# Kernel optimization log

Hardware: AMD Instinct MI355X
Metric: run time of the kernel (lower is better)

Reference implementation:

```python
import jax, jax.numpy as jnp
import numpy as np

CAPACITY_KWH = 13.5
MAX_CHARGE_RATE_KW = 5.0
INITIAL_CHARGE_KWH = 6.75
KW_TO_KWH = 5.0 / 60.0  # 5-minute interval

B, T = 4096, 4096


def setup_inputs() -> dict:
    key = jax.random.key(0)
    k1, k2, k3, k4 = jax.random.split(key, 4)
    return {
        "grid_action": jax.random.normal(k1, (B, T), dtype=jnp.float32),
        "pv_action": jax.random.uniform(k2, (B, T), dtype=jnp.float32),
        "pv_power": jax.random.uniform(k3, (B, T), dtype=jnp.float32),
        "price": jax.random.uniform(k4, (B, T), dtype=jnp.float32),
    }


def _battery_rollout(grid_action, pv_action, pv_power, price):
    # precompute per-step provisional quantities (all [B, T])
    attempted_pv_rate = pv_action * pv_power
    realised_pv_rate = jnp.clip(attempted_pv_rate, 0.0, MAX_CHARGE_RATE_KW)
    prov_pv_amount = realised_pv_rate * KW_TO_KWH
    attempted_grid_rate = grid_action * MAX_CHARGE_RATE_KW

    def step(state, inp):
        ppc, pvp, agr = inp  # each [B]
        after_pv = jnp.clip(state + ppc, 0.0, CAPACITY_KWH)
        realised_pv_amt = after_pv - state
        actual_pv_rate = realised_pv_amt / KW_TO_KWH
        pv_export = realised_pv_amt - pvp * KW_TO_KWH
        realised_grid_rate = jnp.clip(agr, -MAX_CHARGE_RATE_KW,
                                      MAX_CHARGE_RATE_KW - actual_pv_rate)
        new_state = jnp.clip(after_pv + realised_grid_rate * KW_TO_KWH,
                             0.0, CAPACITY_KWH)
        grid_amt = new_state - after_pv
        return new_state, (new_state, grid_amt, pv_export)

    init = jnp.full((grid_action.shape[0],), INITIAL_CHARGE_KWH,
                    dtype=grid_action.dtype)
    xs = (prov_pv_amount.T, pv_power.T, attempted_grid_rate.T)  # [T, B]
    _, (states, grid_amt, pv_export) = jax.lax.scan(step, init, xs)
    trace = jnp.concatenate([init[None, :], states], axis=0).T  # [B, T+1]
    cost = price / 1000.0 * (grid_amt.T + pv_export.T)          # [B, T]
    return trace, cost


def reference(grid_action, pv_action, pv_power, price):
    return _battery_rollout(grid_action, pv_action, pv_power, price)
```

## Files before the change

kernel.cpp:

```cpp
#include <hip/hip_runtime.h>

#define T_STEPS 4096
#define BLOCK   1024
#define CHUNK   4

constexpr float CAP     = 13.5f;
constexpr float MAXR    = 5.0f;
constexpr float S0      = 6.75f;
constexpr float DT      = (float)(5.0 / 60.0);
constexpr float FIVE_DT = 5.0f * DT;
constexpr float BIG     = 3.402823466e+38f;

struct Trip { float d, l, h; };

__device__ __forceinline__ Trip combine(const Trip& p, const Trip& q) {
    Trip r;
    r.d = p.d + q.d;
    r.l = fminf(fmaxf(p.l + q.d, q.l), q.h);
    r.h = fminf(fmaxf(p.h + q.d, q.l), q.h);
    return r;
}

__global__ __launch_bounds__(BLOCK) void battery_kernel(
    const float* __restrict__ ga, const float* __restrict__ pa,
    const float* __restrict__ pp, const float* __restrict__ pr,
    float* __restrict__ trace, float* __restrict__ cost)
{
    const int b    = blockIdx.x;
    const int tid  = threadIdx.x;
    const int lane = tid & 63;
    const int w    = tid >> 6;
    const long long rowOff = (long long)b * T_STEPS;
    const int t0   = tid * CHUNK;

    const float4 g4  = *reinterpret_cast<const float4*>(ga + rowOff + t0);
    const float4 pa4 = *reinterpret_cast<const float4*>(pa + rowOff + t0);
    const float4 pp4 = *reinterpret_cast<const float4*>(pp + rowOff + t0);
    const float4 pr4 = *reinterpret_cast<const float4*>(pr + rowOff + t0);
    const float gaA[4] = {g4.x,  g4.y,  g4.z,  g4.w};
    const float paA[4] = {pa4.x, pa4.y, pa4.z, pa4.w};
    const float ppA[4] = {pp4.x, pp4.y, pp4.z, pp4.w};
    const float prA[4] = {pr4.x, pr4.y, pr4.z, pr4.w};

    Trip acc;
    #pragma unroll
    for (int j = 0; j < CHUNK; ++j) {
        float rate = fminf(fmaxf(paA[j] * ppA[j], 0.0f), MAXR);
        float a    = rate * DT;
        float u    = (gaA[j] * MAXR) * DT;
        float d    = a + fminf(fmaxf(u, -FIVE_DT), FIVE_DT - a);
        float h    = fminf(fmaxf(CAP + u, CAP - FIVE_DT), CAP);
        Trip f = {d, 0.0f, h};
        acc = (j == 0) ? f : combine(acc, f);
    }

    #pragma unroll
    for (int off = 1; off < 64; off <<= 1) {
        Trip p;
        p.d = __shfl_up(acc.d, off);
        p.l = __shfl_up(acc.l, off);
        p.h = __shfl_up(acc.h, off);
        if (lane >= off) acc = combine(p, acc);
    }

    __shared__ float aggD[16], aggL[16], aggH[16];
    if (lane == 63) { aggD[w] = acc.d; aggL[w] = acc.l; aggH[w] = acc.h; }

    Trip ex;
    ex.d = __shfl_up(acc.d, 1);
    ex.l = __shfl_up(acc.l, 1);
    ex.h = __shfl_up(acc.h, 1);
    if (lane == 0) { ex.d = 0.0f; ex.l = -BIG; ex.h = BIG; }

    __syncthreads();

    Trip pre = {0.0f, -BIG, BIG};
    for (int i = 0; i < w; ++i) {
        Trip q = {aggD[i], aggL[i], aggH[i]};
        pre = combine(pre, q);
    }
    Trip tot = combine(pre, ex);
    float s = fminf(fmaxf(S0 + tot.d, tot.l), tot.h);

    float st[CHUNK], ct[CHUNK];
    #pragma unroll
    for (int j = 0; j < CHUNK; ++j) {
        float rate      = fminf(fmaxf(paA[j] * ppA[j], 0.0f), MAXR);
        float ppc       = rate * DT;
        float after_pv  = fminf(fmaxf(s + ppc, 0.0f), CAP);
        float realised  = after_pv - s;
        float apr       = realised / DT;
        float pv_export = realised - ppA[j] * DT;
        float agr       = gaA[j] * MAXR;
        float rgr       = fminf(fmaxf(agr, -MAXR), MAXR - apr);
        float ns        = fminf(fmaxf(after_pv + rgr * DT, 0.0f), CAP);
        float grid_amt  = ns - after_pv;
        st[j] = ns;
        ct[j] = (prA[j] / 1000.0f) * (grid_amt + pv_export);
        s = ns;
    }

    float4 c4; c4.x = ct[0]; c4.y = ct[1]; c4.z = ct[2]; c4.w = ct[3];
    *reinterpret_cast<float4*>(cost + rowOff + t0) = c4;

    __shared__ float tr[T_STEPS];
    float4 s4; s4.x = st[0]; s4.y = st[1]; s4.z = st[2]; s4.w = st[3];
    *reinterpret_cast<float4*>(tr + t0) = s4;
    __syncthreads();

    const long long trBase = (long long)b * (T_STEPS + 1);
    if (tid == 0) trace[trBase] = S0;
    #pragma unroll
    for (int k = 0; k < CHUNK; ++k) {
        int i = tid + k * BLOCK;
        trace[trBase + 1 + i] = tr[i];
    }
}

extern "C" void kernel_launch(void* const* d_in, const int* in_sizes, int n_in,
                              void* d_out, int out_size, void* d_ws, size_t ws_size,
                              hipStream_t stream) {
    const float* ga = (const float*)d_in[0];
    const float* pa = (const float*)d_in[1];
    const float* pp = (const float*)d_in[2];
    const float* pr = (const float*)d_in[3];
    const int B = in_sizes[0] / T_STEPS;
    float* trace = (float*)d_out;
    float* cost  = (float*)d_out + (long long)B * (T_STEPS + 1);
    battery_kernel<<<B, BLOCK, 0, stream>>>(ga, pa, pp, pr, trace, cost);
}
```

Measured before the change: 320.7 us.

## Assign one wavefront per row with tiled sequential scan and register prefetch

Instead of one 1024-thread block per row doing a block-wide scan, each 64-lane wavefront now owns a whole row. It walks the row in tiles of 512 steps, doing a wave-level scan inside each tile and carrying the state from tile to tile. The next tile's inputs are prefetched into registers, and the trace is transposed through padded per-wave LDS so stores coalesce. This removes __syncthreads and the cross-wave aggregate pass, but makes each row's work serial across tiles and raises register pressure.

After: 321.9 us. About the same (+0.4%).

```diff
diff --git a/kernel.cpp b/kernel.cpp
--- a/kernel.cpp
+++ b/kernel.cpp
@@ -1,15 +1,17 @@
 #include <hip/hip_runtime.h>
 
 #define T_STEPS 4096
-#define BLOCK   1024
-#define CHUNK   4
+#define BLOCK   256
+#define CHUNK   8
+#define TILE    (64 * CHUNK)
+#define NTILES  (T_STEPS / TILE)
+#define RPB     (BLOCK / 64)
 
 constexpr float CAP     = 13.5f;
 constexpr float MAXR    = 5.0f;
 constexpr float S0      = 6.75f;
 constexpr float DT      = (float)(5.0 / 60.0);
 constexpr float FIVE_DT = 5.0f * DT;
-constexpr float BIG     = 3.402823466e+38f;
 
 struct Trip { float d, l, h; };
 
@@ -21,99 +23,123 @@
     return r;
 }
 
-__global__ __launch_bounds__(BLOCK) void battery_kernel(
+__global__ __launch_bounds__(BLOCK, 4) void battery_kernel(
     const float* __restrict__ ga, const float* __restrict__ pa,
     const float* __restrict__ pp, const float* __restrict__ pr,
-    float* __restrict__ trace, float* __restrict__ cost)
+    float* __restrict__ trace, float* __restrict__ cost, int B)
 {
-    const int b    = blockIdx.x;
     const int tid  = threadIdx.x;
     const int lane = tid & 63;
-    const int w    = tid >> 6;
-    const long long rowOff = (long long)b * T_STEPS;
-    const int t0   = tid * CHUNK;
+    const int wv   = tid >> 6;
+    const int row  = blockIdx.x * RPB + wv;
 
-    const float4 g4  = *reinterpret_cast<const float4*>(ga + rowOff + t0);
-    const float4 pa4 = *reinterpret_cast<const float4*>(pa + rowOff + t0);
-    const float4 pp4 = *reinterpret_cast<const float4*>(pp + rowOff + t0);
-    const float4 pr4 = *reinterpret_cast<const float4*>(pr + rowOff + t0);
-    const float gaA[4] = {g4.x,  g4.y,  g4.z,  g4.w};
-    const float paA[4] = {pa4.x, pa4.y, pa4.z, pa4.w};
-    const float ppA[4] = {pp4.x, pp4.y, pp4.z, pp4.w};
-    const float prA[4] = {pr4.x, pr4.y, pr4.z, pr4.w};
+    __shared__ float buf[RPB][TILE + TILE / 8];
+    float* sb = buf[wv];
 
-    Trip acc;
-    #pragma unroll
-    for (int j = 0; j < CHUNK; ++j) {
-        float rate = fminf(fmaxf(paA[j] * ppA[j], 0.0f), MAXR);
-        float a    = rate * DT;
-        float u    = (gaA[j] * MAXR) * DT;
-        float d    = a + fminf(fmaxf(u, -FIVE_DT), FIVE_DT - a);
-        float h    = fminf(fmaxf(CAP + u, CAP - FIVE_DT), CAP);
-        Trip f = {d, 0.0f, h};
-        acc = (j == 0) ? f : combine(acc, f);
-    }
+    if (row >= B) return;
 
-    #pragma unroll
-    for (int off = 1; off < 64; off <<= 1) {
-        Trip p;
-        p.d = __shfl_up(acc.d, off);
-        p.l = __shfl_up(acc.l, off);
-        p.h = __shfl_up(acc.h, off);
-        if (lane >= off) acc = combine(p, acc);
-    }
+    const long long rowOff = (long long)row * T_STEPS;
+    const long long trBase = (long long)row * (T_STEPS + 1);
+    const float* gaR = ga + rowOff;
+    const float* paR = pa + rowOff;
+    const float* ppR = pp + rowOff;
+    const float* prR = pr + rowOff;
 
-    __shared__ float aggD[16], aggL[16], aggH[16];
-    if (lane == 63) { aggD[w] = acc.d; aggL[w] = acc.l; aggH[w] = acc.h; }
+    if (lane == 0) trace[trBase] = S0;
 
-    Trip ex;
-    ex.d = __shfl_up(acc.d, 1);
-    ex.l = __shfl_up(acc.l, 1);
-    ex.h = __shfl_up(acc.h, 1);
-    if (lane == 0) { ex.d = 0.0f; ex.l = -BIG; ex.h = BIG; }
+    const int b0 = lane * CHUNK;
+    float4 cg0 = *reinterpret_cast<const float4*>(gaR + b0);
+    float4 cg1 = *reinterpret_cast<const float4*>(gaR + b0 + 4);
+    float4 cp0 = *reinterpret_cast<const float4*>(paR + b0);
+    float4 cp1 = *reinterpret_cast<const float4*>(paR + b0 + 4);
+    float4 cq0 = *reinterpret_cast<const float4*>(ppR + b0);
+    float4 cq1 = *reinterpret_cast<const float4*>(ppR + b0 + 4);
+    float4 cr0 = *reinterpret_cast<const float4*>(prR + b0);
+    float4 cr1 = *reinterpret_cast<const float4*>(prR + b0 + 4);
 
-    __syncthreads();
+    float s = S0;
 
-    Trip pre = {0.0f, -BIG, BIG};
-    for (int i = 0; i < w; ++i) {
-        Trip q = {aggD[i], aggL[i], aggH[i]};
-        pre = combine(pre, q);
-    }
-    Trip tot = combine(pre, ex);
-    float s = fminf(fmaxf(S0 + tot.d, tot.l), tot.h);
+    for (int k = 0; k < NTILES; ++k) {
+        const int kn = (k + 1 < NTILES) ? k + 1 : k;
+        const int nb = kn * TILE + lane * CHUNK;
+        float4 ng0 = *reinterpret_cast<const float4*>(gaR + nb);
+        float4 ng1 = *reinterpret_cast<const float4*>(gaR + nb + 4);
+        float4 np0 = *reinterpret_cast<const float4*>(paR + nb);
+        float4 np1 = *reinterpret_cast<const float4*>(paR + nb + 4);
+        float4 nq0 = *reinterpret_cast<const float4*>(ppR + nb);
+        float4 nq1 = *reinterpret_cast<const float4*>(ppR + nb + 4);
+        float4 nr0 = *reinterpret_cast<const float4*>(prR + nb);
+        float4 nr1 = *reinterpret_cast<const float4*>(prR + nb + 4);
 
-    float st[CHUNK], ct[CHUNK];
-    #pragma unroll
-    for (int j = 0; j < CHUNK; ++j) {
-        float rate      = fminf(fmaxf(paA[j] * ppA[j], 0.0f), MAXR);
-        float ppc       = rate * DT;
-        float after_pv  = fminf(fmaxf(s + ppc, 0.0f), CAP);
-        float realised  = after_pv - s;
-        float apr       = realised / DT;
-        float pv_export = realised - ppA[j] * DT;
-        float agr       = gaA[j] * MAXR;
-        float rgr       = fminf(fmaxf(agr, -MAXR), MAXR - apr);
-        float ns        = fminf(fmaxf(after_pv + rgr * DT, 0.0f), CAP);
-        float grid_amt  = ns - after_pv;
-        st[j] = ns;
-        ct[j] = (prA[j] / 1000.0f) * (grid_amt + pv_export);
-        s = ns;
-    }
+        const float gaA[8] = {cg0.x,cg0.y,cg0.z,cg0.w,cg1.x,cg1.y,cg1.z,cg1.w};
+        const float paA[8] = {cp0.x,cp0.y,cp0.z,cp0.w,cp1.x,cp1.y,cp1.z,cp1.w};
+        const float ppA[8] = {cq0.x,cq0.y,cq0.z,cq0.w,cq1.x,cq1.y,cq1.z,cq1.w};
+        const float prA[8] = {cr0.x,cr0.y,cr0.z,cr0.w,cr1.x,cr1.y,cr1.z,cr1.w};
 
-    float4 c4; c4.x = ct[0]; c4.y = ct[1]; c4.z = ct[2]; c4.w = ct[3];
-    *reinterpret_cast<float4*>(cost + rowOff + t0) = c4;
+        float aA[8], agrA[8];
+        Trip acc;
+        #pragma unroll
+        for (int j = 0; j < CHUNK; ++j) {
+            float rate = fminf(fmaxf(paA[j] * ppA[j], 0.0f), MAXR);
+            float a    = rate * DT;
+            float agr  = gaA[j] * MAXR;
+            float u    = agr * DT;
+            aA[j] = a; agrA[j] = agr;
+            Trip f;
+            f.d = a + fminf(fmaxf(u, -FIVE_DT), FIVE_DT - a);
+            f.l = 0.0f;
+            f.h = fminf(fmaxf(CAP + u, CAP - FIVE_DT), CAP);
+            acc = (j == 0) ? f : combine(acc, f);
+        }
 
-    __shared__ float tr[T_STEPS];
-    float4 s4; s4.x = st[0]; s4.y = st[1]; s4.z = st[2]; s4.w = st[3];
-    *reinterpret_cast<float4*>(tr + t0) = s4;
-    __syncthreads();
+        #pragma unroll
+        for (int off = 1; off < 64; off <<= 1) {
+            Trip p;
+            p.d = __shfl_up(acc.d, off);
+            p.l = __shfl_up(acc.l, off);
+            p.h = __shfl_up(acc.h, off);
+            if (lane >= off) acc = combine(p, acc);
+        }
 
-    const long long trBase = (long long)b * (T_STEPS + 1);
-    if (tid == 0) trace[trBase] = S0;
-    #pragma unroll
-    for (int k = 0; k < CHUNK; ++k) {
-        int i = tid + k * BLOCK;
-        trace[trBase + 1 + i] = tr[i];
+        float exd = __shfl_up(acc.d, 1);
+        float exl = __shfl_up(acc.l, 1);
+        float exh = __shfl_up(acc.h, 1);
+        float scur = fminf(fmaxf(s + exd, exl), exh);
+        if (lane == 0) scur = s;
+
+        float st[8], ct[8];
+        #pragma unroll
+        for (int j = 0; j < CHUNK; ++j) {
+            float after_pv  = fminf(fmaxf(scur + aA[j], 0.0f), CAP);
+            float realised  = after_pv - scur;
+            float apr       = realised / DT;
+            float pv_export = realised - ppA[j] * DT;
+            float rgr       = fminf(fmaxf(agrA[j], -MAXR), MAXR - apr);
+            float ns        = fminf(fmaxf(after_pv + rgr * DT, 0.0f), CAP);
+            float grid_amt  = ns - after_pv;
+            st[j] = ns;
+            ct[j] = (prA[j] / 1000.0f) * (grid_amt + pv_export);
+            scur  = ns;
+        }
+        s = __shfl(scur, 63);
+
+        const long long cb = rowOff + (long long)k * TILE + lane * CHUNK;
+        *reinterpret_cast<float4*>(cost + cb)     = make_float4(ct[0], ct[1], ct[2], ct[3]);
+        *reinterpret_cast<float4*>(cost + cb + 4) = make_float4(ct[4], ct[5], ct[6], ct[7]);
+
+        #pragma unroll
+        for (int j = 0; j < CHUNK; ++j)
+            sb[9 * lane + j] = st[j];
+        __builtin_amdgcn_wave_barrier();
+        const long long tb = trBase + 1 + (long long)k * TILE;
+        #pragma unroll
+        for (int m = 0; m < CHUNK; ++m) {
+            int E = lane + 64 * m;
+            trace[tb + E] = sb[E + (E >> 3)];
+        }
+        __builtin_amdgcn_wave_barrier();
+
+        cg0=ng0; cg1=ng1; cp0=np0; cp1=np1; cq0=nq0; cq1=nq1; cr0=nr0; cr1=nr1;
     }
 }
 
@@ -127,5 +153,6 @@
     const int B = in_sizes[0] / T_STEPS;
     float* trace = (float*)d_out;
     float* cost  = (float*)d_out + (long long)B * (T_STEPS + 1);
-    battery_kernel<<<B, BLOCK, 0, stream>>>(ga, pa, pp, pr, trace, cost);
+    const int grid = (B + RPB - 1) / RPB;
+    battery_kernel<<<grid, BLOCK, 0, stream>>>(ga, pa, pp, pr, trace, cost, B);
 }
```
